# Kernel tuning notes

Hardware: AMD Instinct MI355X
Metric: run time of the kernel (lower is better)

Reference implementation:

```python
import jax, jax.numpy as jnp
import numpy as np

# Dims: B=16 graphs, T=354 timesteps (l_max), N=64 nodes, H=128 model dim, NS=32 complex SSM modes

def setup_inputs() -> dict:
    key = jax.random.key(0)
    ks = jax.random.split(key, 10)
    B, T, N, H, NS = 16, 354, 64, 128, 32
    x = jax.random.normal(ks[0], (B, T, N), jnp.float32)
    W_in = jax.random.normal(ks[1], (H, 1), jnp.float32) * 0.5
    b_in = jnp.zeros((H,), jnp.float32)
    # S4D params: timescales log-uniform in [1e-3, 1e-1], A = -1/2 + i*pi*n (S4D-Lin init)
    log_dt = (jnp.log(0.001) + jax.random.uniform(ks[2], (H,), jnp.float32) * (jnp.log(0.1) - jnp.log(0.001))).astype(jnp.float32)
    A_re = -0.5 * jnp.ones((H, NS), jnp.float32)
    A_im = jnp.broadcast_to(np.pi * jnp.arange(NS, dtype=jnp.float32), (H, NS)).astype(jnp.float32) + 0.0
    C_re = jax.random.normal(ks[3], (H, NS), jnp.float32) * (0.5 ** 0.5)
    C_im = jax.random.normal(ks[4], (H, NS), jnp.float32) * (0.5 ** 0.5)
    D = jax.random.normal(ks[5], (H,), jnp.float32)
    W_out = jax.random.normal(ks[6], (2 * H, H), jnp.float32) * (1.0 / np.sqrt(H))
    b_out = jnp.zeros((2 * H,), jnp.float32)
    W_cls = jax.random.normal(ks[7], (1, H), jnp.float32) * (1.0 / np.sqrt(H))
    b_cls = jnp.zeros((1,), jnp.float32)
    return {"x": x, "W_in": W_in, "b_in": b_in, "log_dt": log_dt, "A_re": A_re, "A_im": A_im,
            "C_re": C_re, "C_im": C_im, "D": D, "W_out": W_out, "b_out": b_out,
            "W_cls": W_cls, "b_cls": b_cls}


def reference(x, W_in, b_in, log_dt, A_re, A_im, C_re, C_im, D, W_out, b_out, W_cls, b_cls):
    B, T, N = x.shape
    H = W_in.shape[0]
    # (B,T,N) -> (B*N, T, 1) per-node scalar series
    u = x.transpose(0, 2, 1).reshape(B * N, T, 1)
    u = u * W_in[:, 0] + b_in            # input_proj: (BN, T, H)
    u = u.transpose(0, 2, 1)             # transposed layout: (BN, H, L)
    # ---- S4D kernel (ZOH discretization, conjugate-pair 2*Re trick) ----
    dt = jnp.exp(log_dt)                 # (H,)
    A = A_re + 1j * A_im                 # (H, NS) complex64
    dtA = A * dt[:, None]                # (H, NS)
    C = C_re + 1j * C_im
    C_disc = C * (jnp.exp(dtA) - 1.0) / A
    l = jnp.arange(T)
    vand = jnp.exp(dtA[:, :, None] * l)  # Vandermonde (H, NS, L)
    K = 2.0 * jnp.real(jnp.einsum('hn,hnl->hl', C_disc, vand))  # (H, L)
    # ---- FFT causal long convolution + skip ----
    n_fft = 2 * T
    yf = jnp.fft.rfft(u, n_fft) * jnp.fft.rfft(K, n_fft)
    y = jnp.fft.irfft(yf, n_fft)[..., :T] + D[:, None] * u   # (BN, H, L)
    y = jax.nn.gelu(y)
    # dropout: identity at inference
    # ---- position-wise output linear H -> 2H, then GLU over channels ----
    g = jnp.einsum('bhl,gh->bgl', y, W_out) + b_out[:, None]  # (BN, 2H, L)
    z = g[:, :H] * jax.nn.sigmoid(g[:, H:])                    # (BN, H, L)
    # ---- pooling + classifier ----
    node_feats = z.mean(axis=-1).reshape(B, N, H)
    graph_feats = node_feats.mean(axis=1)                      # (B, H)
    logits = graph_feats @ W_cls.T + b_cls                     # (B, 1)
    return logits
```

## Files before the change

kernel.cpp:

```cpp
#include <hip/hip_runtime.h>
#include <hip/hip_bf16.h>


#define B_  16
#define T_  354
#define N_  64
#define H_  128
#define NS_ 32
#define BN_ (B_*N_)
#define TP_ 384
#define KW_ 512
#define PAD_ 136
#define GT_ 8
#define NGT_ ((T_ + GT_ - 1) / GT_)
#define WB_ ((2 * H_ * H_) / 512)

typedef __attribute__((ext_vector_type(8))) short bf16x8;
typedef __attribute__((ext_vector_type(4))) float f32x4;

static __device__ __forceinline__ unsigned short f32_to_bf16(float f) {
    unsigned int u = __float_as_uint(f);
    unsigned int r = 0x7FFFu + ((u >> 16) & 1u);
    return (unsigned short)((u + r) >> 16);
}

static __device__ __forceinline__ void gload_lds4(const void* g, void* l) {
    __builtin_amdgcn_global_load_lds(
        (const __attribute__((address_space(1))) unsigned int*)g,
        (__attribute__((address_space(3))) unsigned int*)l, 4, 0, 0);
}

static __device__ __forceinline__ float gelu_f(float v) {
    float v2 = v * v;
    float x  = v * fmaf(0.0713548162726f, v2, 1.5957691216057f);
    float sg = 1.0f / (1.0f + __expf(-x));
    return v * sg;
}

__global__ __launch_bounds__(512) void k_pre(
        const float* __restrict__ log_dt,
        const float* __restrict__ A_re, const float* __restrict__ A_im,
        const float* __restrict__ C_re, const float* __restrict__ C_im,
        const float* __restrict__ b_in, const float* __restrict__ D,
        const float* __restrict__ x, const float* __restrict__ W_out,
        unsigned short* __restrict__ Krev, float* __restrict__ koff,
        unsigned short* __restrict__ xbf, unsigned short* __restrict__ Wbf) {
    const int blk = blockIdx.x;
    const int tid = threadIdx.x;

    if (blk >= H_ + 96) {
        int id = (blk - H_ - 96) * 512 + tid;
        if (id < 2 * H_ * H_) Wbf[id] = f32_to_bf16(W_out[id]);
        return;
    }
    if (blk >= H_) {
        __shared__ float xt[64][68];
        int idx = blk - H_;
        int bt = idx / 6, tt = idx % 6;
        int r  = tid >> 3, fc = tid & 7;
        int t  = tt * 64 + r;
        float4 v0 = make_float4(0.f, 0.f, 0.f, 0.f), v1 = v0;
        if (t < T_) {
            const float* xp = x + ((size_t)bt * T_ + t) * N_ + fc * 8;
            v0 = *(const float4*)xp;
            v1 = *(const float4*)(xp + 4);
        }
        *(float4*)&xt[r][fc * 8]     = v0;
        *(float4*)&xt[r][fc * 8 + 4] = v1;
        __syncthreads();
        int n = tid >> 3, tc = tid & 7;
        unsigned short pk[8];
#pragma unroll
        for (int k = 0; k < 8; k++) pk[k] = f32_to_bf16(xt[tc * 8 + k][n]);
        *(uint4*)(xbf + (size_t)(bt * 64 + n) * TP_ + tt * 64 + tc * 8)
            = *(const uint4*)pk;
        return;
    }

    const int h = blk;
    const int l = tid;
    float val = 0.0f;
    if (l < T_) {
        float dt = expf(log_dt[h]);
        float fl = (float)l;
#pragma unroll 4
        for (int m = 0; m < NS_; m++) {
            float are = A_re[h * NS_ + m], aim = A_im[h * NS_ + m];
            float dre = are * dt, dim = aim * dt;
            float er  = expf(dre);
            float c1, s1; __sincosf(dim, &s1, &c1);
            float e_re = er * c1, e_im = er * s1;
            float m_re = e_re - 1.0f, m_im = e_im;
            float inv  = 1.0f / (are * are + aim * aim);
            float q_re = (m_re * are + m_im * aim) * inv;
            float q_im = (m_im * are - m_re * aim) * inv;
            float c_r = C_re[h * NS_ + m], c_i = C_im[h * NS_ + m];
            float cdre = c_r * q_re - c_i * q_im;
            float cdim = c_r * q_im + c_i * q_re;
            float el = expf(dre * fl);
            float cl, sl; __sincosf(dim * fl, &sl, &cl);
            val += el * (cdre * cl - cdim * sl);
        }
        val *= 2.0f;
        if (l == 0) val += D[h];
    }

    __shared__ float sc[512];
    sc[l] = (l < T_) ? val : 0.0f;
    __syncthreads();
    for (int off = 1; off < 512; off <<= 1) {
        float add = (l >= off) ? sc[l - off] : 0.0f;
        __syncthreads();
        sc[l] += add;
        __syncthreads();
    }

    if (l < T_) {
        koff[l * H_ + h] = b_in[h] * sc[l];
        unsigned short bv = f32_to_bf16(val);
#pragma unroll
        for (int r = 0; r < 8; r++)
            Krev[((size_t)r * H_ + h) * KW_ + (T_ - 1 - l) + r] = bv;
    }
}

__global__ __launch_bounds__(256, 3) void k_conv(
        const unsigned short* __restrict__ xbf,
        const unsigned short* __restrict__ Krev,
        const float* __restrict__ koff,
        const float* __restrict__ W_in,
        unsigned short* __restrict__ Y) {
    __shared__ unsigned short x_lds[64 * PAD_];

    const int tid  = threadIdx.x;
    const int w    = tid >> 6;
    const int lane = tid & 63;
    const int q    = lane >> 4;
    const int l16  = lane & 15;
    const int bn0  = blockIdx.x * 64;
    const int t0   = blockIdx.y * 2;
    const int nkb  = ((t0 + 1) >> 7) + 1;

    float win[2][4];
#pragma unroll
    for (int mt = 0; mt < 2; mt++)
#pragma unroll
        for (int rr = 0; rr < 4; rr++)
            win[mt][rr] = W_in[32 * w + 16 * mt + 4 * q + rr];

    f32x4 cacc[2][2][4];
#pragma unroll
    for (int tt = 0; tt < 2; tt++)
#pragma unroll
        for (int mt = 0; mt < 2; mt++)
#pragma unroll
            for (int nt = 0; nt < 4; nt++)
                cacc[tt][mt][nt] = (f32x4){0.f, 0.f, 0.f, 0.f};

    for (int kb = 0; kb < nkb; kb++) {
        const int tau0 = kb << 7;
        __syncthreads();
#pragma unroll
        for (int i = 0; i < 16; i++) {
            int r = w * 16 + i;
            gload_lds4(xbf + (size_t)(bn0 + r) * TP_ + tau0 + lane * 2,
                       &x_lds[r * PAD_]);
        }
        __syncthreads();

#pragma unroll
        for (int tt = 0; tt < 2; tt++) {
            const int t = t0 + tt;
            if (tau0 > t) continue;
            const int L  = 353 - t + tau0;
            const int cp = (-L) & 7;
            const unsigned short* kbase = Krev + (size_t)cp * H_ * KW_ + (L + cp);

            bf16x8 kf[4][2];
#pragma unroll
            for (int ks = 0; ks < 4; ks++)
#pragma unroll
                for (int mt = 0; mt < 2; mt++)
                    kf[ks][mt] = *(const bf16x8*)(kbase
                        + (size_t)(32 * w + 16 * mt + l16) * KW_ + ks * 32 + q * 8);

#pragma unroll
            for (int ks = 0; ks < 4; ks++) {
                bf16x8 bf[4];
#pragma unroll
                for (int nt = 0; nt < 4; nt++)
                    bf[nt] = *(const bf16x8*)&x_lds[(16 * nt + l16) * PAD_ + ks * 32 + q * 8];
#pragma unroll
                for (int mt = 0; mt < 2; mt++)
#pragma unroll
                    for (int nt = 0; nt < 4; nt++)
                        cacc[tt][mt][nt] = __builtin_amdgcn_mfma_f32_16x16x32_bf16(
                            kf[ks][mt], bf[nt], cacc[tt][mt][nt], 0, 0, 0);
            }
        }
    }

#pragma unroll
    for (int tt = 0; tt < 2; tt++) {
        const int t = t0 + tt;
        __syncthreads();
#pragma unroll
        for (int mt = 0; mt < 2; mt++) {
            int h0 = 32 * w + 16 * mt + 4 * q;
#pragma unroll
            for (int nt = 0; nt < 4; nt++) {
                unsigned short pk[4];
#pragma unroll
                for (int rr = 0; rr < 4; rr++) {
                    float v = fmaf(cacc[tt][mt][nt][rr], win[mt][rr],
                                   koff[t * H_ + h0 + rr]);
                    pk[rr] = f32_to_bf16(gelu_f(v));
                }
                *(uint2*)&x_lds[(16 * nt + l16) * PAD_ + h0] = *(const uint2*)pk;
            }
        }
        __syncthreads();
#pragma unroll
        for (int i = 0; i < 4; i++) {
            int c    = i * 256 + tid;
            int row  = c >> 4;
            int col8 = (c & 15) * 8;
            uint4 v = *(const uint4*)&x_lds[row * PAD_ + col8];
            *(uint4*)(Y + ((size_t)t * BN_ + bn0 + row) * H_ + col8) = v;
        }
    }
}

__global__ __launch_bounds__(256, 4) void k_glu(
        const unsigned short* __restrict__ Y,
        const unsigned short* __restrict__ Wbf,
        const float* __restrict__ b_out,
        float* __restrict__ node_sum) {
    __shared__ unsigned short Yt[64 * PAD_];

    const int tid  = threadIdx.x;
    const int w    = tid >> 6;
    const int lane = tid & 63;
    const int q    = lane >> 4;
    const int l16  = lane & 15;
    const int jg   = blockIdx.x & 1;
    const int bn0  = (blockIdx.x >> 1) * 64;
    const int tg0  = blockIdx.y * GT_;
    const int jlow = jg * 64 + w * 16;
    const int jhigh = jlow + 128;

    bf16x8 wfrag[2][4];
#pragma unroll
    for (int ks = 0; ks < 4; ks++) {
        wfrag[0][ks] = *(const bf16x8*)(Wbf + (size_t)(jlow  + l16) * H_ + ks * 32 + q * 8);
        wfrag[1][ks] = *(const bf16x8*)(Wbf + (size_t)(jhigh + l16) * H_ + ks * 32 + q * 8);
    }
    float bo1[4], bo2[4];
#pragma unroll
    for (int rr = 0; rr < 4; rr++) {
        bo1[rr] = b_out[jlow  + 4 * q + rr];
        bo2[rr] = b_out[jhigh + 4 * q + rr];
    }

    f32x4 zacc[4];
#pragma unroll
    for (int nt = 0; nt < 4; nt++) zacc[nt] = (f32x4){0.f, 0.f, 0.f, 0.f};

    for (int g = 0; g < GT_; g++) {
        const int t = tg0 + g;
        if (t >= T_) break;
        __syncthreads();
#pragma unroll
        for (int i = 0; i < 16; i++) {
            int r = w * 16 + i;
            gload_lds4(Y + ((size_t)t * BN_ + bn0 + r) * H_ + lane * 2,
                       &Yt[r * PAD_]);
        }
        __syncthreads();

        f32x4 gacc[2][4];
#pragma unroll
        for (int mt = 0; mt < 2; mt++)
#pragma unroll
            for (int nt = 0; nt < 4; nt++) gacc[mt][nt] = (f32x4){0.f, 0.f, 0.f, 0.f};

#pragma unroll
        for (int ks = 0; ks < 4; ks++) {
            bf16x8 yf[4];
#pragma unroll
            for (int nt = 0; nt < 4; nt++)
                yf[nt] = *(const bf16x8*)&Yt[(16 * nt + l16) * PAD_ + ks * 32 + q * 8];
#pragma unroll
            for (int mt = 0; mt < 2; mt++)
#pragma unroll
                for (int nt = 0; nt < 4; nt++)
                    gacc[mt][nt] = __builtin_amdgcn_mfma_f32_16x16x32_bf16(
                        wfrag[mt][ks], yf[nt], gacc[mt][nt], 0, 0, 0);
        }

#pragma unroll
        for (int nt = 0; nt < 4; nt++)
#pragma unroll
            for (int rr = 0; rr < 4; rr++) {
                float a  = gacc[0][nt][rr] + bo1[rr];
                float bs = gacc[1][nt][rr] + bo2[rr];
                float sg = 1.0f / (1.0f + __expf(-bs));
                zacc[nt][rr] += a * sg;
            }
    }

#pragma unroll
    for (int nt = 0; nt < 4; nt++)
#pragma unroll
        for (int rr = 0; rr < 4; rr++) {
            int bn = bn0 + 16 * nt + l16;
            int j  = jlow + 4 * q + rr;
            atomicAdd(&node_sum[bn * H_ + j], zacc[nt][rr]);
        }
}

__global__ void k_cls(const float* __restrict__ node_sum,
                      const float* __restrict__ W_cls, const float* __restrict__ b_cls,
                      float* __restrict__ out) {
    const int b = blockIdx.x, tid = threadIdx.x;
    float s = 0.0f;
    for (int i = tid; i < N_ * H_; i += 256)
        s += node_sum[b * (N_ * H_) + i] * W_cls[i & (H_ - 1)];
    __shared__ float red[256];
    red[tid] = s;
    __syncthreads();
    for (int off = 128; off > 0; off >>= 1) {
        if (tid < off) red[tid] += red[tid + off];
        __syncthreads();
    }
    if (tid == 0) out[b] = red[0] * (1.0f / (354.0f * 64.0f)) + b_cls[0];
}

extern "C" void kernel_launch(void* const* d_in, const int* in_sizes, int n_in,
                              void* d_out, int out_size, void* d_ws, size_t ws_size,
                              hipStream_t stream) {
    const float* x      = (const float*)d_in[0];
    const float* W_in   = (const float*)d_in[1];
    const float* b_in   = (const float*)d_in[2];
    const float* log_dt = (const float*)d_in[3];
    const float* A_re   = (const float*)d_in[4];
    const float* A_im   = (const float*)d_in[5];
    const float* C_re   = (const float*)d_in[6];
    const float* C_im   = (const float*)d_in[7];
    const float* D      = (const float*)d_in[8];
    const float* W_out  = (const float*)d_in[9];
    const float* b_out  = (const float*)d_in[10];
    const float* W_cls  = (const float*)d_in[11];
    const float* b_cls  = (const float*)d_in[12];

    char* ws = (char*)d_ws;
    float*          node_sum = (float*)(ws + 0);
    unsigned short* Krev     = (unsigned short*)(ws + 524288);
    float*          koff     = (float*)(ws + 1572864);
    unsigned short* xbf      = (unsigned short*)(ws + 1754112);
    unsigned short* Wbf      = (unsigned short*)(ws + 2540544);
    unsigned short* Y        = (unsigned short*)(ws + 2606080);

    hipMemsetAsync(ws, 0, 1572864, stream);
    k_pre<<<dim3(H_ + 96 + WB_), dim3(512), 0, stream>>>(
        log_dt, A_re, A_im, C_re, C_im, b_in, D, x, W_out, Krev, koff, xbf, Wbf);
    k_conv<<<dim3(BN_ / 64, T_ / 2), dim3(256), 0, stream>>>(
        xbf, Krev, koff, W_in, Y);
    k_glu<<<dim3(2 * BN_ / 64, NGT_), dim3(256), 0, stream>>>(
        Y, Wbf, b_out, node_sum);
    k_cls<<<dim3(B_), dim3(256), 0, stream>>>(node_sum, W_cls, b_cls, (float*)d_out);
}
```

Before: 281.3 us.

## Double-buffer LDS tiles in conv and GLU kernels, enlarge GLU time group

Both the convolution and GLU kernels now use two LDS buffers. The next tile's global-to-LDS load is issued before computing on the current tile, and one barrier per iteration is dropped. The GLU kernel's time-group size doubles, so each block keeps its weight fragments for more timesteps and the grid shrinks. The extra LDS buffer can lower occupancy, and the larger time group leaves fewer blocks to fill the device.

```diff
diff --git a/kernel.cpp b/kernel.cpp
--- a/kernel.cpp
+++ b/kernel.cpp
@@ -11,7 +11,7 @@
 #define TP_ 384
 #define KW_ 512
 #define PAD_ 136
-#define GT_ 8
+#define GT_ 16
 #define NGT_ ((T_ + GT_ - 1) / GT_)
 #define WB_ ((2 * H_ * H_) / 512)
 
@@ -130,7 +130,7 @@
         const float* __restrict__ koff,
         const float* __restrict__ W_in,
         unsigned short* __restrict__ Y) {
-    __shared__ unsigned short x_lds[64 * PAD_];
+    __shared__ unsigned short x_lds[2][64 * PAD_];
 
     const int tid  = threadIdx.x;
     const int w    = tid >> 6;
@@ -139,7 +139,7 @@
     const int l16  = lane & 15;
     const int bn0  = blockIdx.x * 64;
     const int t0   = blockIdx.y * 2;
-    const int nkb  = ((t0 + 1) >> 7) + 1;
+    const int nkb  = (t0 >> 7) + 1;
 
     float win[2][4];
 #pragma unroll
@@ -157,21 +157,30 @@
             for (int nt = 0; nt < 4; nt++)
                 cacc[tt][mt][nt] = (f32x4){0.f, 0.f, 0.f, 0.f};
 
+#pragma unroll
+    for (int i = 0; i < 16; i++) {
+        int r = w * 16 + i;
+        gload_lds4(xbf + (size_t)(bn0 + r) * TP_ + lane * 2,
+                   &x_lds[0][r * PAD_]);
+    }
+
     for (int kb = 0; kb < nkb; kb++) {
         const int tau0 = kb << 7;
         __syncthreads();
-#pragma unroll
-        for (int i = 0; i < 16; i++) {
-            int r = w * 16 + i;
-            gload_lds4(xbf + (size_t)(bn0 + r) * TP_ + tau0 + lane * 2,
-                       &x_lds[r * PAD_]);
-        }
-        __syncthreads();
+        if (kb + 1 < nkb) {
+            const int taun = (kb + 1) << 7;
+#pragma unroll
+            for (int i = 0; i < 16; i++) {
+                int r = w * 16 + i;
+                gload_lds4(xbf + (size_t)(bn0 + r) * TP_ + taun + lane * 2,
+                           &x_lds[(kb + 1) & 1][r * PAD_]);
+            }
+        }
+        const unsigned short* xb = x_lds[kb & 1];
 
 #pragma unroll
         for (int tt = 0; tt < 2; tt++) {
-            const int t = t0 + tt;
-            if (tau0 > t) continue;
+            const int t  = t0 + tt;
             const int L  = 353 - t + tau0;
             const int cp = (-L) & 7;
             const unsigned short* kbase = Krev + (size_t)cp * H_ * KW_ + (L + cp);
@@ -189,7 +198,7 @@
                 bf16x8 bf[4];
 #pragma unroll
                 for (int nt = 0; nt < 4; nt++)
-                    bf[nt] = *(const bf16x8*)&x_lds[(16 * nt + l16) * PAD_ + ks * 32 + q * 8];
+                    bf[nt] = *(const bf16x8*)&xb[(16 * nt + l16) * PAD_ + ks * 32 + q * 8];
 #pragma unroll
                 for (int mt = 0; mt < 2; mt++)
 #pragma unroll
@@ -216,7 +225,7 @@
                                    koff[t * H_ + h0 + rr]);
                     pk[rr] = f32_to_bf16(gelu_f(v));
                 }
-                *(uint2*)&x_lds[(16 * nt + l16) * PAD_ + h0] = *(const uint2*)pk;
+                *(uint2*)&x_lds[0][(16 * nt + l16) * PAD_ + h0] = *(const uint2*)pk;
             }
         }
         __syncthreads();
@@ -225,7 +234,7 @@
             int c    = i * 256 + tid;
             int row  = c >> 4;
             int col8 = (c & 15) * 8;
-            uint4 v = *(const uint4*)&x_lds[row * PAD_ + col8];
+            uint4 v = *(const uint4*)&x_lds[0][row * PAD_ + col8];
             *(uint4*)(Y + ((size_t)t * BN_ + bn0 + row) * H_ + col8) = v;
         }
     }
@@ -236,7 +245,7 @@
         const unsigned short* __restrict__ Wbf,
         const float* __restrict__ b_out,
         float* __restrict__ node_sum) {
-    __shared__ unsigned short Yt[64 * PAD_];
+    __shared__ unsigned short Yt[2][64 * PAD_];
 
     const int tid  = threadIdx.x;
     const int w    = tid >> 6;
@@ -266,17 +275,26 @@
 #pragma unroll
     for (int nt = 0; nt < 4; nt++) zacc[nt] = (f32x4){0.f, 0.f, 0.f, 0.f};
 
+#pragma unroll
+    for (int i = 0; i < 16; i++) {
+        int r = w * 16 + i;
+        gload_lds4(Y + ((size_t)tg0 * BN_ + bn0 + r) * H_ + lane * 2,
+                   &Yt[0][r * PAD_]);
+    }
+
     for (int g = 0; g < GT_; g++) {
         const int t = tg0 + g;
         if (t >= T_) break;
         __syncthreads();
-#pragma unroll
-        for (int i = 0; i < 16; i++) {
-            int r = w * 16 + i;
-            gload_lds4(Y + ((size_t)t * BN_ + bn0 + r) * H_ + lane * 2,
-                       &Yt[r * PAD_]);
-        }
-        __syncthreads();
+        if (g + 1 < GT_ && t + 1 < T_) {
+#pragma unroll
+            for (int i = 0; i < 16; i++) {
+                int r = w * 16 + i;
+                gload_lds4(Y + ((size_t)(t + 1) * BN_ + bn0 + r) * H_ + lane * 2,
+                           &Yt[(g + 1) & 1][r * PAD_]);
+            }
+        }
+        const unsigned short* buf = Yt[g & 1];
 
         f32x4 gacc[2][4];
 #pragma unroll
@@ -289,7 +307,7 @@
             bf16x8 yf[4];
 #pragma unroll
             for (int nt = 0; nt < 4; nt++)
-                yf[nt] = *(const bf16x8*)&Yt[(16 * nt + l16) * PAD_ + ks * 32 + q * 8];
+                yf[nt] = *(const bf16x8*)&buf[(16 * nt + l16) * PAD_ + ks * 32 + q * 8];
 #pragma unroll
             for (int mt = 0; mt < 2; mt++)
 #pragma unroll
```

Measured after the change: 257.4 us. -8.5%, faster.
